# Optimization experiments

Measured on AMD Instinct MI355X. Metric: run time of the kernel, lower is better.

## Reference

```python
import jax, jax.numpy as jnp
import numpy as np

ALPHA = (0.02, 0.04, 0.08, 0.16)
CHAMFER_W, SMOOTH_W, CURVATURE_W = 1.0, 1.0, 0.3
NS = (8192, 4096, 2048, 1024)
B = 2


def _sqdist(a, b):
    # a: [B,N,3], b: [B,M,3] -> [B,N,M] squared euclidean distance
    return (jnp.sum(a * a, axis=-1)[:, :, None]
            - 2.0 * jnp.einsum('bnc,bmc->bnm', a, b)
            + jnp.sum(b * b, axis=-1)[:, None, :])


def _knn(d, k):
    # k smallest distances + indices along last axis
    neg, idx = jax.lax.top_k(-d, k)
    return -neg, idx


def _gather(points, idx):
    # points: [B,M,C], idx: [B,N,K] -> [B,N,K,C]
    return jax.vmap(lambda p, i: p[i])(points, idx)


def _scale_loss(pc1, pc2, flow):
    # pc1, pc2, flow: [B,3,N]-like -> permute to points-last layout
    p1 = jnp.transpose(pc1, (0, 2, 1))   # [B,N,3]
    p2 = jnp.transpose(pc2, (0, 2, 1))   # [B,M,3]
    fl = jnp.transpose(flow, (0, 2, 1))  # [B,N,3]
    warp = p1 + fl                        # warped pc1

    # curvature of pc2 (10-NN on pc2 itself)
    _, k22 = _knn(_sqdist(p2, p2), 10)
    cv2 = jnp.sum(_gather(p2, k22) - p2[:, :, None, :], axis=2) / 9.0  # [B,M,3]

    # 10-NN on pc1 (shared for warped curvature and smoothness; 9-NN is prefix)
    _, k11 = _knn(_sqdist(p1, p1), 10)
    cvw = jnp.sum(_gather(warp, k11) - warp[:, :, None, :], axis=2) / 9.0  # [B,N,3]

    k9 = k11[:, :, :9]
    gfl = _gather(fl, k9)  # [B,N,9,3]
    smooth = jnp.sum(jnp.linalg.norm(gfl - fl[:, :, None, :], axis=3), axis=2) / 8.0  # [B,N]

    # chamfer between warped pc1 and pc2
    d12 = _sqdist(warp, p2)               # [B,N,M]
    dist1 = jnp.min(d12, axis=-1)         # [B,N]
    dist2 = jnp.min(d12, axis=1)          # [B,M]

    # inverse-distance interpolation of pc2 curvature onto warped pc1 (5-NN)
    dist, kidx = _knn(d12, 5)             # [B,N,5]
    gcv = _gather(cv2, kidx)              # [B,N,5,3]
    w = 1.0 / (dist + 1e-8)
    w = w / jnp.sum(w, axis=2, keepdims=True)
    inter = jnp.sum(w[..., None] * gcv, axis=2)  # [B,N,3]

    chamfer = jnp.mean(jnp.sum(dist1, axis=1)) + jnp.mean(jnp.sum(dist2, axis=1))
    smoothness = jnp.mean(jnp.sum(smooth, axis=1))
    curv = jnp.mean(jnp.sum(jnp.sum((inter - cvw) ** 2, axis=2), axis=1))
    return chamfer, smoothness, curv


def setup_inputs() -> dict:
    key = jax.random.key(0)
    keys = jax.random.split(key, 12)
    out = {}
    names = ['pc1', 'pc2', 'flow']
    k = 0
    for name in names:
        for i, n in enumerate(NS):
            scale = 1.0 if name != 'flow' else 0.1
            out[f'{name}_{i}'] = scale * jax.random.normal(keys[k], (B, 3, n), dtype=jnp.float32)
            k += 1
    return out


def reference(pc1_0, pc1_1, pc1_2, pc1_3,
              pc2_0, pc2_1, pc2_2, pc2_3,
              flow_0, flow_1, flow_2, flow_3):
    pcs1 = (pc1_0, pc1_1, pc1_2, pc1_3)
    pcs2 = (pc2_0, pc2_1, pc2_2, pc2_3)
    flows = (flow_0, flow_1, flow_2, flow_3)
    ch = sm = cv = jnp.float32(0.0)
    for a, p1, p2, fl in zip(ALPHA, pcs1, pcs2, flows):
        c, s, k = _scale_loss(p1, p2, fl)
        ch = ch + a * c
        sm = sm + a * s
        cv = cv + a * k
    total = CHAMFER_W * ch + CURVATURE_W * cv + SMOOTH_W * sm
    return jnp.reshape(total, (1,))
```

## Files before the change

kernel.cpp:

```cpp
#include <hip/hip_runtime.h>
#include <math.h>


#define BLOCK 512
#define UNIT 1024
#define NTOT 15360
#define MASKC 0xFFFFE000u
#define PB 340

typedef unsigned int uint;
typedef __attribute__((ext_vector_type(8))) float f8;

struct Params {
  const float* pc1[4];
  const float* pc2[4];
  const float* fl[4];
  float4* cv2;
  float4* cvw;
  float* keys;
  float* out;
};

__device__ __forceinline__ void decode(int r, int wv, int& s, int& b,
                                       int& i0, int& lo, int& N, int& cpw,
                                       int& off, float& alpha) {
  int rr;
  if (r < 256)      { s = 0; rr = r; }
  else if (r < 320) { s = 1; rr = r - 256; }
  else if (r < 336) { s = 2; rr = r - 320; }
  else              { s = 3; rr = r - 336; }
  N = 8192 >> s;
  cpw = 8 >> s;
  int perb = 128 >> (2 * s);
  b = rr >> (7 - 2 * s);
  int chunk = rr & (perb - 1);
  int qg = (chunk << s) + (wv >> (3 - s));
  i0 = qg << 6;
  lo = (wv & (cpw - 1)) << 10;
  off = 16384 - (16384 >> s);
  alpha = 0.02f * (float)(1 << s);
}

__device__ __forceinline__ float wave_sum(float v) {
  #pragma unroll
  for (int o = 32; o; o >>= 1) v += __shfl_down(v, o, 64);
  return v;
}

template <int K>
__device__ __forceinline__ void key_insert(float (&kd)[K], float kf) {
  #pragma unroll
  for (int m = K - 1; m >= 1; --m)
    kd[m] = __builtin_amdgcn_fmed3f(kf, kd[m - 1], kd[m]);
  kd[0] = fminf(kd[0], kf);
}

template <int K>
__device__ __forceinline__ void merge_pair(float (&a)[K], const float (&b)[K]) {
  #pragma unroll
  for (int m = 0; m < K; ++m) key_insert<K>(a, b[m]);
}

__device__ __forceinline__ float pack_key_u(float d, uint iw) {
  return __uint_as_float((__float_as_uint(d) & MASKC) | iw);
}

__device__ __forceinline__ void sload3(const float* px, const float* py,
                                       const float* pz, int boff,
                                       f8& x, f8& y, f8& z) {
  asm volatile(
      "s_load_dwordx8 %0, %3, %6\n\t"
      "s_load_dwordx8 %1, %4, %6\n\t"
      "s_load_dwordx8 %2, %5, %6\n\t"
      "s_waitcnt lgkmcnt(0)"
      : "=&s"(x), "=&s"(y), "=&s"(z)
      : "s"(px), "s"(py), "s"(pz), "s"(boff));
}

__device__ __forceinline__ void sload6(const float* px, const float* py,
                                       const float* pz, const float* fx,
                                       const float* fy, const float* fz,
                                       int boff, f8& x, f8& y, f8& z,
                                       f8& u, f8& v, f8& w) {
  asm volatile(
      "s_load_dwordx8 %0, %6, %12\n\t"
      "s_load_dwordx8 %1, %7, %12\n\t"
      "s_load_dwordx8 %2, %8, %12\n\t"
      "s_load_dwordx8 %3, %9, %12\n\t"
      "s_load_dwordx8 %4, %10, %12\n\t"
      "s_load_dwordx8 %5, %11, %12\n\t"
      "s_waitcnt lgkmcnt(0)"
      : "=&s"(x), "=&s"(y), "=&s"(z), "=&s"(u), "=&s"(v), "=&s"(w)
      : "s"(px), "s"(py), "s"(pz), "s"(fx), "s"(fy), "s"(fz), "s"(boff));
}

template <int K>
__device__ void scan_k(const float* px, const float* py, const float* pz,
                       int lo_u, float ax, float ay, float az,
                       float (&a)[K], float (&b)[K]) {
  #pragma unroll 1
  for (int c0 = 0; c0 < UNIT; c0 += 8) {
    f8 xs, ys, zs;
    sload3(px, py, pz, (lo_u + c0) * 4, xs, ys, zs);
    #pragma unroll
    for (int t = 0; t < 8; t += 2) {
      float dxa = xs[t] - ax, dya = ys[t] - ay, dza = zs[t] - az;
      float dA = fmaf(dxa, dxa, fmaf(dya, dya, dza * dza));
      float dxb = xs[t + 1] - ax, dyb = ys[t + 1] - ay, dzb = zs[t + 1] - az;
      float dB = fmaf(dxb, dxb, fmaf(dyb, dyb, dzb * dzb));
      key_insert<K>(a, pack_key_u(dA, (uint)(lo_u + c0 + t)));
      key_insert<K>(b, pack_key_u(dB, (uint)(lo_u + c0 + t + 1)));
    }
  }
}

__device__ void scan_w(const float* px, const float* py, const float* pz,
                       const float* fx, const float* fy, const float* fz,
                       int lo_u, float ax, float ay, float az,
                       float (&a)[1], float (&b)[1]) {
  #pragma unroll 1
  for (int c0 = 0; c0 < UNIT; c0 += 8) {
    f8 xs, ys, zs, us, vs, ws;
    sload6(px, py, pz, fx, fy, fz, (lo_u + c0) * 4, xs, ys, zs, us, vs, ws);
    #pragma unroll
    for (int t = 0; t < 8; t += 2) {
      float cxa = xs[t] + us[t], cya = ys[t] + vs[t], cza = zs[t] + ws[t];
      float dxa = cxa - ax, dya = cya - ay, dza = cza - az;
      float dA = fmaf(dxa, dxa, fmaf(dya, dya, dza * dza));
      float cxb = xs[t + 1] + us[t + 1], cyb = ys[t + 1] + vs[t + 1],
            czb = zs[t + 1] + ws[t + 1];
      float dxb = cxb - ax, dyb = cyb - ay, dzb = czb - az;
      float dB = fmaf(dxb, dxb, fmaf(dyb, dyb, dzb * dzb));
      a[0] = fminf(a[0], dA);
      b[0] = fminf(b[0], dB);
    }
  }
}

template <int K>
__device__ __forceinline__ bool merge_group(float (&a)[K], float* sm,
                                            int tid, int cpw) {
  const int STR = K | 1;
  int q = tid & 63, wv = tid >> 6;
  #pragma unroll
  for (int m = 0; m < K; ++m) sm[(wv * 64 + q) * STR + m] = a[m];
  __syncthreads();
  if (wv & (cpw - 1)) return false;
  for (int w = wv + 1; w < wv + cpw; ++w)
    #pragma unroll
    for (int m = 0; m < K; ++m)
      key_insert<K>(a, sm[(w * 64 + q) * STR + m]);
  return true;
}

__global__ __launch_bounds__(1) void k_zero(float* out) { out[0] = 0.f; }

__global__ __launch_bounds__(BLOCK, 8) void k_fused(Params P) {
  __shared__ float sm[8 * 64 * 11];
  int tid = threadIdx.x, q = tid & 63, wv = tid >> 6;
  int pass = blockIdx.x / PB, r = blockIdx.x % PB;
  int s, b, i0, lo, N, cpw, off; float alpha;
  decode(r, wv, s, b, i0, lo, N, cpw, off, alpha);
  int i = i0 + q;
  int lo_u = __builtin_amdgcn_readfirstlane(lo);

  if (pass == 0) {
    const float* p2 = P.pc2[s] + b * 3 * N;
    float ax = p2[i], ay = p2[N + i], az = p2[2 * N + i];
    float a[10], bb[10];
    #pragma unroll
    for (int m = 0; m < 10; ++m) { a[m] = 3.0e38f; bb[m] = 3.0e38f; }
    scan_k<10>(p2, p2 + N, p2 + 2 * N, lo_u, ax, ay, az, a, bb);
    merge_pair<10>(a, bb);
    if (!merge_group<10>(a, sm, tid, cpw)) return;
    float sx = 0.f, sy = 0.f, sz = 0.f;
    #pragma unroll
    for (int m = 0; m < 10; ++m) {
      int j = (int)(__float_as_uint(a[m]) & 0x1FFFu);
      sx += p2[j]; sy += p2[N + j]; sz += p2[2 * N + j];
    }
    const float inv9 = 1.f / 9.f;
    P.cv2[b * NTOT + off + i] = make_float4((sx - 10.f * ax) * inv9,
                                            (sy - 10.f * ay) * inv9,
                                            (sz - 10.f * az) * inv9, 0.f);
  } else if (pass == 1) {
    const float* p1 = P.pc1[s] + b * 3 * N;
    const float* fl = P.fl[s] + b * 3 * N;
    float ax = p1[i], ay = p1[N + i], az = p1[2 * N + i];
    float a[10], bb[10];
    #pragma unroll
    for (int m = 0; m < 10; ++m) { a[m] = 3.0e38f; bb[m] = 3.0e38f; }
    scan_k<10>(p1, p1 + N, p1 + 2 * N, lo_u, ax, ay, az, a, bb);
    merge_pair<10>(a, bb);
    if (!merge_group<10>(a, sm, tid, cpw)) return;
    float fix = fl[i], fiy = fl[N + i], fiz = fl[2 * N + i];
    float wix = ax + fix, wiy = ay + fiy, wiz = az + fiz;
    float sx = 0.f, sy = 0.f, sz = 0.f, smooth = 0.f;
    float dmax = -1.f, worst = 0.f;
    #pragma unroll
    for (int m = 0; m < 10; ++m) {
      int j = (int)(__float_as_uint(a[m]) & 0x1FFFu);
      float px = p1[j], py = p1[N + j], pz = p1[2 * N + j];
      float flx = fl[j], fly = fl[N + j], flz = fl[2 * N + j];
      sx += px + flx; sy += py + fly; sz += pz + flz;
      float ddx = px - ax, ddy = py - ay, ddz = pz - az;
      float d = fmaf(ddx, ddx, fmaf(ddy, ddy, ddz * ddz));
      float gx = flx - fix, gy = fly - fiy, gz = flz - fiz;
      float term = sqrtf(fmaf(gx, gx, fmaf(gy, gy, gz * gz)));
      smooth += term;
      if (d > dmax) { dmax = d; worst = term; }
    }
    smooth -= worst;
    const float inv9 = 1.f / 9.f;
    P.cvw[b * NTOT + off + i] = make_float4((sx - 10.f * wix) * inv9,
                                            (sy - 10.f * wiy) * inv9,
                                            (sz - 10.f * wiz) * inv9, 0.f);
    float ssum = wave_sum(smooth * (1.f / 8.f));
    if (q == 0) atomicAdd(P.out, alpha * 0.5f * ssum);
  } else if (pass == 2) {
    const float* p1 = P.pc1[s] + b * 3 * N;
    const float* fl = P.fl[s] + b * 3 * N;
    const float* p2 = P.pc2[s] + b * 3 * N;
    float ax = p2[i], ay = p2[N + i], az = p2[2 * N + i];
    float a[1], bb[1];
    a[0] = 3.0e38f; bb[0] = 3.0e38f;
    scan_w(p1, p1 + N, p1 + 2 * N, fl, fl + N, fl + 2 * N,
           lo_u, ax, ay, az, a, bb);
    merge_pair<1>(a, bb);
    if (!merge_group<1>(a, sm, tid, cpw)) return;
    float msum = wave_sum(a[0]);
    if (q == 0) atomicAdd(P.out, alpha * 0.5f * msum);
  } else {
    const float* p1 = P.pc1[s] + b * 3 * N;
    const float* fl = P.fl[s] + b * 3 * N;
    const float* p2 = P.pc2[s] + b * 3 * N;
    float ax = p1[i] + fl[i], ay = p1[N + i] + fl[N + i],
          az = p1[2 * N + i] + fl[2 * N + i];
    float a[5], bb[5];
    #pragma unroll
    for (int m = 0; m < 5; ++m) { a[m] = 3.0e38f; bb[m] = 3.0e38f; }
    scan_k<5>(p2, p2 + N, p2 + 2 * N, lo_u, ax, ay, az, a, bb);
    merge_pair<5>(a, bb);
    if (!merge_group<5>(a, sm, tid, cpw)) return;
    #pragma unroll
    for (int m = 0; m < 5; ++m)
      P.keys[m * (2 * NTOT) + b * NTOT + off + i] = a[m];
  }
}

__global__ __launch_bounds__(256) void k_epi(Params P) {
  int t = blockIdx.x * 256 + threadIdx.x;
  int b = t >= NTOT;
  int r = t - b * NTOT;
  int s, i;
  if (r < 8192)       { s = 0; i = r; }
  else if (r < 12288) { s = 1; i = r - 8192; }
  else if (r < 14336) { s = 2; i = r - 12288; }
  else                { s = 3; i = r - 14336; }
  int N = 8192 >> s;
  int off = 16384 - (16384 >> s);
  float alpha = 0.02f * (float)(1 << s);
  const float* p1 = P.pc1[s] + b * 3 * N;
  const float* fl = P.fl[s] + b * 3 * N;
  const float* p2 = P.pc2[s] + b * 3 * N;
  float ax = p1[i] + fl[i], ay = p1[N + i] + fl[N + i],
        az = p1[2 * N + i] + fl[2 * N + i];
  float dist1 = 3.0e38f, wsum = 0.f, ix = 0.f, iy = 0.f, iz = 0.f;
  #pragma unroll
  for (int m = 0; m < 5; ++m) {
    uint key = __float_as_uint(P.keys[m * (2 * NTOT) + b * NTOT + off + i]);
    int j = (int)(key & 0x1FFFu);
    float px = p2[j], py = p2[N + j], pz = p2[2 * N + j];
    float ddx = px - ax, ddy = py - ay, ddz = pz - az;
    float d = fmaf(ddx, ddx, fmaf(ddy, ddy, ddz * ddz));
    dist1 = fminf(dist1, d);
    float w = 1.f / (d + 1e-8f);
    wsum += w;
    float4 cv = P.cv2[b * NTOT + off + j];
    ix += w * cv.x; iy += w * cv.y; iz += w * cv.z;
  }
  float inv = 1.f / wsum;
  ix *= inv; iy *= inv; iz *= inv;
  float4 cw = P.cvw[b * NTOT + off + i];
  float ex = ix - cw.x, ey = iy - cw.y, ez = iz - cw.z;
  float curv = fmaf(ex, ex, fmaf(ey, ey, ez * ez));
  float v = alpha * 0.5f * (dist1 + 0.3f * curv);
  v = wave_sum(v);
  if ((threadIdx.x & 63) == 0) atomicAdd(P.out, v);
}

extern "C" void kernel_launch(void* const* d_in, const int* in_sizes, int n_in,
                              void* d_out, int out_size, void* d_ws,
                              size_t ws_size, hipStream_t stream) {
  Params P;
  for (int s = 0; s < 4; ++s) {
    P.pc1[s] = (const float*)d_in[s];
    P.pc2[s] = (const float*)d_in[4 + s];
    P.fl[s]  = (const float*)d_in[8 + s];
  }
  P.cv2 = (float4*)d_ws;
  P.cvw = (float4*)((char*)d_ws + (size_t)2 * NTOT * sizeof(float4));
  P.keys = (float*)((char*)d_ws + (size_t)4 * NTOT * sizeof(float4));
  P.out = (float*)d_out;

  k_zero<<<dim3(1), dim3(1), 0, stream>>>(P.out);
  k_fused<<<dim3(4 * PB), dim3(BLOCK), 0, stream>>>(P);
  k_epi<<<dim3((2 * NTOT) / 256), dim3(256), 0, stream>>>(P);
}
```

Before: 315.2 us.

## Replace fused block-merge kernel with atomic work-queue wave tasks and split epilogues

Adds a persistent-style scan kernel in which each wave pulls a task from an atomic counter. A task covers one of four passes (pc2 self-kNN, pc1 self-kNN, warp-to-pc2 5-NN, pc2-to-warp min) over a 1024-point column slice, and partial top-K lists go to global workspace instead of being merged in shared memory. Two epilogue kernels then merge the partials and compute curvature, smoothness and chamfer terms, and the distance math is written with 2-wide vector FMAs. This aims to balance load across scales and drop block-level syncs. The cost is extra global traffic for the partial keys, an extra launch, and a path that only runs when the workspace is large enough.

```diff
diff --git a/kernel.cpp b/kernel.cpp
--- a/kernel.cpp
+++ b/kernel.cpp
@@ -2,14 +2,17 @@
 #include <math.h>
 
 
-#define BLOCK 512
 #define UNIT 1024
 #define NTOT 15360
 #define MASKC 0xFFFFE000u
 #define PB 340
+#define BLOCK 512
+#define NTASKS 10880
+#define TOTS 174080
 
 typedef unsigned int uint;
 typedef __attribute__((ext_vector_type(8))) float f8;
+typedef __attribute__((ext_vector_type(2))) float f2;
 
 struct Params {
   const float* pc1[4];
@@ -17,9 +20,315 @@
   const float* fl[4];
   float4* cv2;
   float4* cvw;
+  float* k0;
+  float* k1;
+  float* k3;
+  uint* d2u;
+  uint* cnt;
   float* keys;
   float* out;
 };
+
+
+__device__ __forceinline__ float wave_sum(float v) {
+  #pragma unroll
+  for (int o = 32; o; o >>= 1) v += __shfl_down(v, o, 64);
+  return v;
+}
+
+template <int K>
+__device__ __forceinline__ void key_insert(float (&kd)[K], float kf) {
+  #pragma unroll
+  for (int m = K - 1; m >= 1; --m)
+    kd[m] = __builtin_amdgcn_fmed3f(kf, kd[m - 1], kd[m]);
+  kd[0] = fminf(kd[0], kf);
+}
+
+template <int K>
+__device__ __forceinline__ void merge_pair(float (&a)[K], const float (&b)[K]) {
+  #pragma unroll
+  for (int m = 0; m < K; ++m) key_insert<K>(a, b[m]);
+}
+
+__device__ __forceinline__ void sload3(const float* px, const float* py,
+                                       const float* pz, int boff,
+                                       f8& x, f8& y, f8& z) {
+  asm volatile(
+      "s_load_dwordx8 %0, %3, %6\n\t"
+      "s_load_dwordx8 %1, %4, %6\n\t"
+      "s_load_dwordx8 %2, %5, %6\n\t"
+      "s_waitcnt lgkmcnt(0)"
+      : "=&s"(x), "=&s"(y), "=&s"(z)
+      : "s"(px), "s"(py), "s"(pz), "s"(boff));
+}
+
+__device__ __forceinline__ void sload6(const float* px, const float* py,
+                                       const float* pz, const float* fx,
+                                       const float* fy, const float* fz,
+                                       int boff, f8& x, f8& y, f8& z,
+                                       f8& u, f8& v, f8& w) {
+  asm volatile(
+      "s_load_dwordx8 %0, %6, %12\n\t"
+      "s_load_dwordx8 %1, %7, %12\n\t"
+      "s_load_dwordx8 %2, %8, %12\n\t"
+      "s_load_dwordx8 %3, %9, %12\n\t"
+      "s_load_dwordx8 %4, %10, %12\n\t"
+      "s_load_dwordx8 %5, %11, %12\n\t"
+      "s_waitcnt lgkmcnt(0)"
+      : "=&s"(x), "=&s"(y), "=&s"(z), "=&s"(u), "=&s"(v), "=&s"(w)
+      : "s"(px), "s"(py), "s"(pz), "s"(fx), "s"(fy), "s"(fz), "s"(boff));
+}
+
+template <int K>
+__device__ void scan_k(const float* px, const float* py, const float* pz,
+                       int lo, float ax, float ay, float az,
+                       float (&a)[K], float (&b)[K]) {
+  f2 qx = {ax, ax}, qy = {ay, ay}, qz = {az, az};
+  #pragma unroll 1
+  for (int c0 = 0; c0 < UNIT; c0 += 8) {
+    f8 xs, ys, zs;
+    sload3(px, py, pz, (lo + c0) * 4, xs, ys, zs);
+    #pragma unroll
+    for (int t = 0; t < 8; t += 2) {
+      f2 dx = f2{xs[t], xs[t + 1]} - qx;
+      f2 dy = f2{ys[t], ys[t + 1]} - qy;
+      f2 dz = f2{zs[t], zs[t + 1]} - qz;
+      f2 d = __builtin_elementwise_fma(
+          dx, dx, __builtin_elementwise_fma(dy, dy, dz * dz));
+      uint i0 = (uint)(lo + c0 + t);
+      key_insert<K>(a, __uint_as_float((__float_as_uint(d.x) & MASKC) | i0));
+      key_insert<K>(b,
+                    __uint_as_float((__float_as_uint(d.y) & MASKC) | (i0 + 1)));
+    }
+  }
+}
+
+__device__ void scan_w(const float* px, const float* py, const float* pz,
+                       const float* fx, const float* fy, const float* fz,
+                       int lo, float ax, float ay, float az,
+                       float (&a)[1], float (&b)[1]) {
+  #pragma unroll 1
+  for (int c0 = 0; c0 < UNIT; c0 += 8) {
+    f8 xs, ys, zs, us, vs, ws;
+    sload6(px, py, pz, fx, fy, fz, (lo + c0) * 4, xs, ys, zs, us, vs, ws);
+    #pragma unroll
+    for (int t = 0; t < 8; t += 2) {
+      float cxa = xs[t] + us[t], cya = ys[t] + vs[t], cza = zs[t] + ws[t];
+      float dxa = cxa - ax, dya = cya - ay, dza = cza - az;
+      float dA = fmaf(dxa, dxa, fmaf(dya, dya, dza * dza));
+      float cxb = xs[t + 1] + us[t + 1], cyb = ys[t + 1] + vs[t + 1],
+            czb = zs[t + 1] + ws[t + 1];
+      float dxb = cxb - ax, dyb = cyb - ay, dzb = czb - az;
+      float dB = fmaf(dxb, dxb, fmaf(dyb, dyb, dzb * dzb));
+      a[0] = fminf(a[0], dA);
+      b[0] = fminf(b[0], dB);
+    }
+  }
+}
+
+
+__global__ __launch_bounds__(256) void k_init(Params P) {
+  int t = blockIdx.x * 256 + threadIdx.x;
+  if (t == 0) { P.out[0] = 0.f; *P.cnt = 0u; }
+  if (t < 2 * NTOT) P.d2u[t] = 0x7F7FFFFFu;
+}
+
+__global__ __launch_bounds__(256, 8) void k_scan(Params P) {
+  int lane = threadIdx.x & 63;
+  for (;;) {
+    uint t;
+    if (lane == 0) t = atomicAdd(P.cnt, 1u);
+    t = (uint)__builtin_amdgcn_readfirstlane(__shfl((int)t, 0, 64));
+    if (t >= NTASKS) return;
+    int p = t / 2720, u = t % 2720;
+    int s, part, g;
+    if (u < 2048)      { s = 0; part = u & 7; g = u >> 3; }
+    else if (u < 2560) { s = 1; u -= 2048; part = u & 3; g = u >> 2; }
+    else if (u < 2688) { s = 2; u -= 2560; part = u & 1; g = u >> 1; }
+    else               { s = 3; u -= 2688; part = 0; g = u; }
+    int gpb = 128 >> s;
+    int b = g >> (7 - s), qg = g & (gpb - 1);
+    int N = 8192 >> s, i = qg * 64 + lane, lo = part << 10;
+    int off = 16384 - (16384 >> s);
+    int qid = b * NTOT + off + i;
+    int sb = (s == 0) ? 0 : (s == 1) ? 131072 : (s == 2) ? 163840 : 172032;
+    int slot = sb + part * 2 * N + b * N + i;
+
+    if (p == 0) {
+      const float* p2 = P.pc2[s] + b * 3 * N;
+      float ax = p2[i], ay = p2[N + i], az = p2[2 * N + i];
+      float a[10], bb[10];
+      #pragma unroll
+      for (int m = 0; m < 10; ++m) { a[m] = 3.0e38f; bb[m] = 3.0e38f; }
+      scan_k<10>(p2, p2 + N, p2 + 2 * N, lo, ax, ay, az, a, bb);
+      merge_pair<10>(a, bb);
+      #pragma unroll
+      for (int m = 0; m < 10; ++m) P.k0[m * TOTS + slot] = a[m];
+    } else if (p == 1) {
+      const float* p1 = P.pc1[s] + b * 3 * N;
+      float ax = p1[i], ay = p1[N + i], az = p1[2 * N + i];
+      float a[10], bb[10];
+      #pragma unroll
+      for (int m = 0; m < 10; ++m) { a[m] = 3.0e38f; bb[m] = 3.0e38f; }
+      scan_k<10>(p1, p1 + N, p1 + 2 * N, lo, ax, ay, az, a, bb);
+      merge_pair<10>(a, bb);
+      #pragma unroll
+      for (int m = 0; m < 10; ++m) P.k1[m * TOTS + slot] = a[m];
+    } else if (p == 2) {
+      const float* p1 = P.pc1[s] + b * 3 * N;
+      const float* fl = P.fl[s] + b * 3 * N;
+      const float* p2 = P.pc2[s] + b * 3 * N;
+      float ax = p1[i] + fl[i], ay = p1[N + i] + fl[N + i],
+            az = p1[2 * N + i] + fl[2 * N + i];
+      float a[5], bb[5];
+      #pragma unroll
+      for (int m = 0; m < 5; ++m) { a[m] = 3.0e38f; bb[m] = 3.0e38f; }
+      scan_k<5>(p2, p2 + N, p2 + 2 * N, lo, ax, ay, az, a, bb);
+      merge_pair<5>(a, bb);
+      #pragma unroll
+      for (int m = 0; m < 5; ++m) P.k3[m * TOTS + slot] = a[m];
+    } else {
+      const float* p1 = P.pc1[s] + b * 3 * N;
+      const float* fl = P.fl[s] + b * 3 * N;
+      const float* p2 = P.pc2[s] + b * 3 * N;
+      float ax = p2[i], ay = p2[N + i], az = p2[2 * N + i];
+      float a[1], bb[1];
+      a[0] = 3.0e38f; bb[0] = 3.0e38f;
+      scan_w(p1, p1 + N, p1 + 2 * N, fl, fl + N, fl + 2 * N,
+             lo, ax, ay, az, a, bb);
+      atomicMin(P.d2u + qid, __float_as_uint(fminf(a[0], bb[0])));
+    }
+  }
+}
+
+__global__ __launch_bounds__(256) void k_epi_a(Params P) {
+  int t = blockIdx.x * 256 + threadIdx.x;
+  int bq = t >= NTOT;
+  int r = t - bq * NTOT;
+  int s, i;
+  if (r < 8192)       { s = 0; i = r; }
+  else if (r < 12288) { s = 1; i = r - 8192; }
+  else if (r < 14336) { s = 2; i = r - 12288; }
+  else                { s = 3; i = r - 14336; }
+  int N = 8192 >> s;
+  int off = 16384 - (16384 >> s);
+  float alpha = 0.02f * (float)(1 << s);
+  int sb = (s == 0) ? 0 : (s == 1) ? 131072 : (s == 2) ? 163840 : 172032;
+  int slot0 = sb + bq * N + i, stride = 2 * N, parts = 8 >> s;
+  const float inv9 = 1.f / 9.f;
+
+  const float* p2 = P.pc2[s] + bq * 3 * N;
+  {
+    float ax = p2[i], ay = p2[N + i], az = p2[2 * N + i];
+    float a[10];
+    #pragma unroll
+    for (int m = 0; m < 10; ++m) a[m] = 3.0e38f;
+    for (int part = 0; part < parts; ++part)
+      #pragma unroll
+      for (int m = 0; m < 10; ++m)
+        key_insert<10>(a, P.k0[m * TOTS + slot0 + part * stride]);
+    float sx = 0.f, sy = 0.f, sz = 0.f;
+    #pragma unroll
+    for (int m = 0; m < 10; ++m) {
+      int j = (int)(__float_as_uint(a[m]) & 0x1FFFu);
+      sx += p2[j]; sy += p2[N + j]; sz += p2[2 * N + j];
+    }
+    P.cv2[bq * NTOT + off + i] = make_float4((sx - 10.f * ax) * inv9,
+                                             (sy - 10.f * ay) * inv9,
+                                             (sz - 10.f * az) * inv9, 0.f);
+  }
+
+  {
+    const float* p1 = P.pc1[s] + bq * 3 * N;
+    const float* fl = P.fl[s] + bq * 3 * N;
+    float ax = p1[i], ay = p1[N + i], az = p1[2 * N + i];
+    float a[10];
+    #pragma unroll
+    for (int m = 0; m < 10; ++m) a[m] = 3.0e38f;
+    for (int part = 0; part < parts; ++part)
+      #pragma unroll
+      for (int m = 0; m < 10; ++m)
+        key_insert<10>(a, P.k1[m * TOTS + slot0 + part * stride]);
+    float fix = fl[i], fiy = fl[N + i], fiz = fl[2 * N + i];
+    float wix = ax + fix, wiy = ay + fiy, wiz = az + fiz;
+    float sx = 0.f, sy = 0.f, sz = 0.f, smooth = 0.f;
+    float dmax = -1.f, worst = 0.f;
+    #pragma unroll
+    for (int m = 0; m < 10; ++m) {
+      int j = (int)(__float_as_uint(a[m]) & 0x1FFFu);
+      float px = p1[j], py = p1[N + j], pz = p1[2 * N + j];
+      float flx = fl[j], fly = fl[N + j], flz = fl[2 * N + j];
+      sx += px + flx; sy += py + fly; sz += pz + flz;
+      float ddx = px - ax, ddy = py - ay, ddz = pz - az;
+      float d = fmaf(ddx, ddx, fmaf(ddy, ddy, ddz * ddz));
+      float gx = flx - fix, gy = fly - fiy, gz = flz - fiz;
+      float term = sqrtf(fmaf(gx, gx, fmaf(gy, gy, gz * gz)));
+      smooth += term;
+      if (d > dmax) { dmax = d; worst = term; }
+    }
+    smooth -= worst;
+    P.cvw[bq * NTOT + off + i] = make_float4((sx - 10.f * wix) * inv9,
+                                             (sy - 10.f * wiy) * inv9,
+                                             (sz - 10.f * wiz) * inv9, 0.f);
+    float ssum = wave_sum(smooth * (1.f / 8.f));
+    if ((threadIdx.x & 63) == 0) atomicAdd(P.out, alpha * 0.5f * ssum);
+  }
+
+  {
+    float dm = __uint_as_float(P.d2u[t]);
+    float msum = wave_sum(dm);
+    if ((threadIdx.x & 63) == 0) atomicAdd(P.out, alpha * 0.5f * msum);
+  }
+}
+
+__global__ __launch_bounds__(256) void k_epi_b(Params P) {
+  int t = blockIdx.x * 256 + threadIdx.x;
+  int bq = t >= NTOT;
+  int r = t - bq * NTOT;
+  int s, i;
+  if (r < 8192)       { s = 0; i = r; }
+  else if (r < 12288) { s = 1; i = r - 8192; }
+  else if (r < 14336) { s = 2; i = r - 12288; }
+  else                { s = 3; i = r - 14336; }
+  int N = 8192 >> s;
+  int off = 16384 - (16384 >> s);
+  float alpha = 0.02f * (float)(1 << s);
+  int sb = (s == 0) ? 0 : (s == 1) ? 131072 : (s == 2) ? 163840 : 172032;
+  int slot0 = sb + bq * N + i, stride = 2 * N, parts = 8 >> s;
+  const float* p1 = P.pc1[s] + bq * 3 * N;
+  const float* fl = P.fl[s] + bq * 3 * N;
+  const float* p2 = P.pc2[s] + bq * 3 * N;
+  float ax = p1[i] + fl[i], ay = p1[N + i] + fl[N + i],
+        az = p1[2 * N + i] + fl[2 * N + i];
+  float a[5];
+  #pragma unroll
+  for (int m = 0; m < 5; ++m) a[m] = 3.0e38f;
+  for (int part = 0; part < parts; ++part)
+    #pragma unroll
+    for (int m = 0; m < 5; ++m)
+      key_insert<5>(a, P.k3[m * TOTS + slot0 + part * stride]);
+  float dist1 = 3.0e38f, wsum = 0.f, ix = 0.f, iy = 0.f, iz = 0.f;
+  #pragma unroll
+  for (int m = 0; m < 5; ++m) {
+    int j = (int)(__float_as_uint(a[m]) & 0x1FFFu);
+    float px = p2[j], py = p2[N + j], pz = p2[2 * N + j];
+    float ddx = px - ax, ddy = py - ay, ddz = pz - az;
+    float d = fmaf(ddx, ddx, fmaf(ddy, ddy, ddz * ddz));
+    dist1 = fminf(dist1, d);
+    float w = 1.f / (d + 1e-8f);
+    wsum += w;
+    float4 cv = P.cv2[bq * NTOT + off + j];
+    ix += w * cv.x; iy += w * cv.y; iz += w * cv.z;
+  }
+  float inv = 1.f / wsum;
+  ix *= inv; iy *= inv; iz *= inv;
+  float4 cw = P.cvw[bq * NTOT + off + i];
+  float ex = ix - cw.x, ey = iy - cw.y, ez = iz - cw.z;
+  float curv = fmaf(ex, ex, fmaf(ey, ey, ez * ez));
+  float v = wave_sum(dist1 + 0.3f * curv);
+  if ((threadIdx.x & 63) == 0) atomicAdd(P.out, alpha * 0.5f * v);
+}
+
 
 __device__ __forceinline__ void decode(int r, int wv, int& s, int& b,
                                        int& i0, int& lo, int& N, int& cpw,
@@ -39,102 +348,6 @@
   lo = (wv & (cpw - 1)) << 10;
   off = 16384 - (16384 >> s);
   alpha = 0.02f * (float)(1 << s);
-}
-
-__device__ __forceinline__ float wave_sum(float v) {
-  #pragma unroll
-  for (int o = 32; o; o >>= 1) v += __shfl_down(v, o, 64);
-  return v;
-}
-
-template <int K>
-__device__ __forceinline__ void key_insert(float (&kd)[K], float kf) {
-  #pragma unroll
-  for (int m = K - 1; m >= 1; --m)
-    kd[m] = __builtin_amdgcn_fmed3f(kf, kd[m - 1], kd[m]);
-  kd[0] = fminf(kd[0], kf);
-}
-
-template <int K>
-__device__ __forceinline__ void merge_pair(float (&a)[K], const float (&b)[K]) {
-  #pragma unroll
-  for (int m = 0; m < K; ++m) key_insert<K>(a, b[m]);
-}
-
-__device__ __forceinline__ float pack_key_u(float d, uint iw) {
-  return __uint_as_float((__float_as_uint(d) & MASKC) | iw);
-}
-
-__device__ __forceinline__ void sload3(const float* px, const float* py,
-                                       const float* pz, int boff,
-                                       f8& x, f8& y, f8& z) {
-  asm volatile(
-      "s_load_dwordx8 %0, %3, %6\n\t"
-      "s_load_dwordx8 %1, %4, %6\n\t"
-      "s_load_dwordx8 %2, %5, %6\n\t"
-      "s_waitcnt lgkmcnt(0)"
-      : "=&s"(x), "=&s"(y), "=&s"(z)
-      : "s"(px), "s"(py), "s"(pz), "s"(boff));
-}
-
-__device__ __forceinline__ void sload6(const float* px, const float* py,
-                                       const float* pz, const float* fx,
-                                       const float* fy, const float* fz,
-                                       int boff, f8& x, f8& y, f8& z,
-                                       f8& u, f8& v, f8& w) {
-  asm volatile(
-      "s_load_dwordx8 %0, %6, %12\n\t"
-      "s_load_dwordx8 %1, %7, %12\n\t"
-      "s_load_dwordx8 %2, %8, %12\n\t"
-      "s_load_dwordx8 %3, %9, %12\n\t"
-      "s_load_dwordx8 %4, %10, %12\n\t"
-      "s_load_dwordx8 %5, %11, %12\n\t"
-      "s_waitcnt lgkmcnt(0)"
-      : "=&s"(x), "=&s"(y), "=&s"(z), "=&s"(u), "=&s"(v), "=&s"(w)
-      : "s"(px), "s"(py), "s"(pz), "s"(fx), "s"(fy), "s"(fz), "s"(boff));
-}
-
-template <int K>
-__device__ void scan_k(const float* px, const float* py, const float* pz,
-                       int lo_u, float ax, float ay, float az,
-                       float (&a)[K], float (&b)[K]) {
-  #pragma unroll 1
-  for (int c0 = 0; c0 < UNIT; c0 += 8) {
-    f8 xs, ys, zs;
-    sload3(px, py, pz, (lo_u + c0) * 4, xs, ys, zs);
-    #pragma unroll
-    for (int t = 0; t < 8; t += 2) {
-      float dxa = xs[t] - ax, dya = ys[t] - ay, dza = zs[t] - az;
-      float dA = fmaf(dxa, dxa, fmaf(dya, dya, dza * dza));
-      float dxb = xs[t + 1] - ax, dyb = ys[t + 1] - ay, dzb = zs[t + 1] - az;
-      float dB = fmaf(dxb, dxb, fmaf(dyb, dyb, dzb * dzb));
-      key_insert<K>(a, pack_key_u(dA, (uint)(lo_u + c0 + t)));
-      key_insert<K>(b, pack_key_u(dB, (uint)(lo_u + c0 + t + 1)));
-    }
-  }
-}
-
-__device__ void scan_w(const float* px, const float* py, const float* pz,
-                       const float* fx, const float* fy, const float* fz,
-                       int lo_u, float ax, float ay, float az,
-                       float (&a)[1], float (&b)[1]) {
-  #pragma unroll 1
-  for (int c0 = 0; c0 < UNIT; c0 += 8) {
-    f8 xs, ys, zs, us, vs, ws;
-    sload6(px, py, pz, fx, fy, fz, (lo_u + c0) * 4, xs, ys, zs, us, vs, ws);
-    #pragma unroll
-    for (int t = 0; t < 8; t += 2) {
-      float cxa = xs[t] + us[t], cya = ys[t] + vs[t], cza = zs[t] + ws[t];
-      float dxa = cxa - ax, dya = cya - ay, dza = cza - az;
-      float dA = fmaf(dxa, dxa, fmaf(dya, dya, dza * dza));
-      float cxb = xs[t + 1] + us[t + 1], cyb = ys[t + 1] + vs[t + 1],
-            czb = zs[t + 1] + ws[t + 1];
-      float dxb = cxb - ax, dyb = cyb - ay, dzb = czb - az;
-      float dB = fmaf(dxb, dxb, fmaf(dyb, dyb, dzb * dzb));
-      a[0] = fminf(a[0], dA);
-      b[0] = fminf(b[0], dB);
-    }
-  }
 }
 
 template <int K>
@@ -284,9 +497,8 @@
   float4 cw = P.cvw[b * NTOT + off + i];
   float ex = ix - cw.x, ey = iy - cw.y, ez = iz - cw.z;
   float curv = fmaf(ex, ex, fmaf(ey, ey, ez * ez));
-  float v = alpha * 0.5f * (dist1 + 0.3f * curv);
-  v = wave_sum(v);
-  if ((threadIdx.x & 63) == 0) atomicAdd(P.out, v);
+  float v = wave_sum(dist1 + 0.3f * curv);
+  if ((threadIdx.x & 63) == 0) atomicAdd(P.out, alpha * 0.5f * v);
 }
 
 extern "C" void kernel_launch(void* const* d_in, const int* in_sizes, int n_in,
@@ -298,12 +510,25 @@
     P.pc2[s] = (const float*)d_in[4 + s];
     P.fl[s]  = (const float*)d_in[8 + s];
   }
-  P.cv2 = (float4*)d_ws;
-  P.cvw = (float4*)((char*)d_ws + (size_t)2 * NTOT * sizeof(float4));
-  P.keys = (float*)((char*)d_ws + (size_t)4 * NTOT * sizeof(float4));
+  char* ws = (char*)d_ws;
+  P.cv2 = (float4*)ws;
+  P.cvw = (float4*)(ws + 491520);
+  P.k0  = (float*)(ws + 983040);
+  P.k1  = (float*)(ws + 7946240);
+  P.k3  = (float*)(ws + 14909440);
+  P.d2u = (uint*)(ws + 18391040);
+  P.cnt = (uint*)(ws + 18513920);
+  P.keys = (float*)(ws + 983040);
   P.out = (float*)d_out;
 
-  k_zero<<<dim3(1), dim3(1), 0, stream>>>(P.out);
-  k_fused<<<dim3(4 * PB), dim3(BLOCK), 0, stream>>>(P);
-  k_epi<<<dim3((2 * NTOT) / 256), dim3(256), 0, stream>>>(P);
-}
+  if (ws_size >= 18513928) {
+    k_init<<<dim3(120), dim3(256), 0, stream>>>(P);
+    k_scan<<<dim3(2048), dim3(256), 0, stream>>>(P);
+    k_epi_a<<<dim3(120), dim3(256), 0, stream>>>(P);
+    k_epi_b<<<dim3(120), dim3(256), 0, stream>>>(P);
+  } else {
+    k_zero<<<dim3(1), dim3(1), 0, stream>>>(P.out);
+    k_fused<<<dim3(4 * PB), dim3(BLOCK), 0, stream>>>(P);
+    k_epi<<<dim3((2 * NTOT) / 256), dim3(256), 0, stream>>>(P);
+  }
+}
```

Result: slower. 476.3 us (+51.1%).

## Use persistent blocks with atomic task queue and atomicMin-split chamfer reverse pass

Applied to the files above, without the earlier changes.

Replaces the fixed 1360-block launch with 1024 persistent blocks that pull task indices from a global atomic counter. The three kNN passes stay as before, but the reverse chamfer pass is split into finer 256-column slices whose per-point minima are combined with atomicMin on uint-encoded floats and summed in the epilogue. The goal is better load balance and less tail imbalance across CUs. The cost is extra atomics, an init kernel, and a block-wide sync per task.

```diff
diff --git a/kernel.cpp b/kernel.cpp
--- a/kernel.cpp
+++ b/kernel.cpp
@@ -2,11 +2,10 @@
 #include <math.h>
 
 
-#define BLOCK 512
 #define UNIT 1024
 #define NTOT 15360
 #define MASKC 0xFFFFE000u
-#define PB 340
+#define NTASK 2380u
 
 typedef unsigned int uint;
 typedef __attribute__((ext_vector_type(8))) float f8;
@@ -18,8 +17,107 @@
   float4* cv2;
   float4* cvw;
   float* keys;
+  uint* d2u;
+  uint* cnt;
   float* out;
 };
+
+
+__device__ __forceinline__ float wave_sum(float v) {
+  #pragma unroll
+  for (int o = 32; o; o >>= 1) v += __shfl_down(v, o, 64);
+  return v;
+}
+
+template <int K>
+__device__ __forceinline__ void key_insert(float (&kd)[K], float kf) {
+  #pragma unroll
+  for (int m = K - 1; m >= 1; --m)
+    kd[m] = __builtin_amdgcn_fmed3f(kf, kd[m - 1], kd[m]);
+  kd[0] = fminf(kd[0], kf);
+}
+
+template <int K>
+__device__ __forceinline__ void merge_pair(float (&a)[K], const float (&b)[K]) {
+  #pragma unroll
+  for (int m = 0; m < K; ++m) key_insert<K>(a, b[m]);
+}
+
+__device__ __forceinline__ float pack_key_u(float d, uint iw) {
+  return __uint_as_float((__float_as_uint(d) & MASKC) | iw);
+}
+
+__device__ __forceinline__ void sload3(const float* px, const float* py,
+                                       const float* pz, int boff,
+                                       f8& x, f8& y, f8& z) {
+  asm volatile(
+      "s_load_dwordx8 %0, %3, %6\n\t"
+      "s_load_dwordx8 %1, %4, %6\n\t"
+      "s_load_dwordx8 %2, %5, %6\n\t"
+      "s_waitcnt lgkmcnt(0)"
+      : "=&s"(x), "=&s"(y), "=&s"(z)
+      : "s"(px), "s"(py), "s"(pz), "s"(boff));
+}
+
+__device__ __forceinline__ void sload6(const float* px, const float* py,
+                                       const float* pz, const float* fx,
+                                       const float* fy, const float* fz,
+                                       int boff, f8& x, f8& y, f8& z,
+                                       f8& u, f8& v, f8& w) {
+  asm volatile(
+      "s_load_dwordx8 %0, %6, %12\n\t"
+      "s_load_dwordx8 %1, %7, %12\n\t"
+      "s_load_dwordx8 %2, %8, %12\n\t"
+      "s_load_dwordx8 %3, %9, %12\n\t"
+      "s_load_dwordx8 %4, %10, %12\n\t"
+      "s_load_dwordx8 %5, %11, %12\n\t"
+      "s_waitcnt lgkmcnt(0)"
+      : "=&s"(x), "=&s"(y), "=&s"(z), "=&s"(u), "=&s"(v), "=&s"(w)
+      : "s"(px), "s"(py), "s"(pz), "s"(fx), "s"(fy), "s"(fz), "s"(boff));
+}
+
+template <int K>
+__device__ void scan_k(const float* px, const float* py, const float* pz,
+                       int lo, float ax, float ay, float az,
+                       float (&a)[K], float (&b)[K]) {
+  #pragma unroll 1
+  for (int c0 = 0; c0 < UNIT; c0 += 8) {
+    f8 xs, ys, zs;
+    sload3(px, py, pz, (lo + c0) * 4, xs, ys, zs);
+    #pragma unroll
+    for (int t = 0; t < 8; t += 2) {
+      float dxa = xs[t] - ax, dya = ys[t] - ay, dza = zs[t] - az;
+      float dA = fmaf(dxa, dxa, fmaf(dya, dya, dza * dza));
+      float dxb = xs[t + 1] - ax, dyb = ys[t + 1] - ay, dzb = zs[t + 1] - az;
+      float dB = fmaf(dxb, dxb, fmaf(dyb, dyb, dzb * dzb));
+      key_insert<K>(a, pack_key_u(dA, (uint)(lo + c0 + t)));
+      key_insert<K>(b, pack_key_u(dB, (uint)(lo + c0 + t + 1)));
+    }
+  }
+}
+
+__device__ void scan_w256(const float* px, const float* py, const float* pz,
+                          const float* fx, const float* fy, const float* fz,
+                          int lo, float ax, float ay, float az,
+                          float& a0, float& b0) {
+  #pragma unroll 1
+  for (int c0 = 0; c0 < 256; c0 += 8) {
+    f8 xs, ys, zs, us, vs, ws;
+    sload6(px, py, pz, fx, fy, fz, (lo + c0) * 4, xs, ys, zs, us, vs, ws);
+    #pragma unroll
+    for (int t = 0; t < 8; t += 2) {
+      float cxa = xs[t] + us[t], cya = ys[t] + vs[t], cza = zs[t] + ws[t];
+      float dxa = cxa - ax, dya = cya - ay, dza = cza - az;
+      float dA = fmaf(dxa, dxa, fmaf(dya, dya, dza * dza));
+      float cxb = xs[t + 1] + us[t + 1], cyb = ys[t + 1] + vs[t + 1],
+            czb = zs[t + 1] + ws[t + 1];
+      float dxb = cxb - ax, dyb = cyb - ay, dzb = czb - az;
+      float dB = fmaf(dxb, dxb, fmaf(dyb, dyb, dzb * dzb));
+      a0 = fminf(a0, dA);
+      b0 = fminf(b0, dB);
+    }
+  }
+}
 
 __device__ __forceinline__ void decode(int r, int wv, int& s, int& b,
                                        int& i0, int& lo, int& N, int& cpw,
@@ -41,102 +139,6 @@
   alpha = 0.02f * (float)(1 << s);
 }
 
-__device__ __forceinline__ float wave_sum(float v) {
-  #pragma unroll
-  for (int o = 32; o; o >>= 1) v += __shfl_down(v, o, 64);
-  return v;
-}
-
-template <int K>
-__device__ __forceinline__ void key_insert(float (&kd)[K], float kf) {
-  #pragma unroll
-  for (int m = K - 1; m >= 1; --m)
-    kd[m] = __builtin_amdgcn_fmed3f(kf, kd[m - 1], kd[m]);
-  kd[0] = fminf(kd[0], kf);
-}
-
-template <int K>
-__device__ __forceinline__ void merge_pair(float (&a)[K], const float (&b)[K]) {
-  #pragma unroll
-  for (int m = 0; m < K; ++m) key_insert<K>(a, b[m]);
-}
-
-__device__ __forceinline__ float pack_key_u(float d, uint iw) {
-  return __uint_as_float((__float_as_uint(d) & MASKC) | iw);
-}
-
-__device__ __forceinline__ void sload3(const float* px, const float* py,
-                                       const float* pz, int boff,
-                                       f8& x, f8& y, f8& z) {
-  asm volatile(
-      "s_load_dwordx8 %0, %3, %6\n\t"
-      "s_load_dwordx8 %1, %4, %6\n\t"
-      "s_load_dwordx8 %2, %5, %6\n\t"
-      "s_waitcnt lgkmcnt(0)"
-      : "=&s"(x), "=&s"(y), "=&s"(z)
-      : "s"(px), "s"(py), "s"(pz), "s"(boff));
-}
-
-__device__ __forceinline__ void sload6(const float* px, const float* py,
-                                       const float* pz, const float* fx,
-                                       const float* fy, const float* fz,
-                                       int boff, f8& x, f8& y, f8& z,
-                                       f8& u, f8& v, f8& w) {
-  asm volatile(
-      "s_load_dwordx8 %0, %6, %12\n\t"
-      "s_load_dwordx8 %1, %7, %12\n\t"
-      "s_load_dwordx8 %2, %8, %12\n\t"
-      "s_load_dwordx8 %3, %9, %12\n\t"
-      "s_load_dwordx8 %4, %10, %12\n\t"
-      "s_load_dwordx8 %5, %11, %12\n\t"
-      "s_waitcnt lgkmcnt(0)"
-      : "=&s"(x), "=&s"(y), "=&s"(z), "=&s"(u), "=&s"(v), "=&s"(w)
-      : "s"(px), "s"(py), "s"(pz), "s"(fx), "s"(fy), "s"(fz), "s"(boff));
-}
-
-template <int K>
-__device__ void scan_k(const float* px, const float* py, const float* pz,
-                       int lo_u, float ax, float ay, float az,
-                       float (&a)[K], float (&b)[K]) {
-  #pragma unroll 1
-  for (int c0 = 0; c0 < UNIT; c0 += 8) {
-    f8 xs, ys, zs;
-    sload3(px, py, pz, (lo_u + c0) * 4, xs, ys, zs);
-    #pragma unroll
-    for (int t = 0; t < 8; t += 2) {
-      float dxa = xs[t] - ax, dya = ys[t] - ay, dza = zs[t] - az;
-      float dA = fmaf(dxa, dxa, fmaf(dya, dya, dza * dza));
-      float dxb = xs[t + 1] - ax, dyb = ys[t + 1] - ay, dzb = zs[t + 1] - az;
-      float dB = fmaf(dxb, dxb, fmaf(dyb, dyb, dzb * dzb));
-      key_insert<K>(a, pack_key_u(dA, (uint)(lo_u + c0 + t)));
-      key_insert<K>(b, pack_key_u(dB, (uint)(lo_u + c0 + t + 1)));
-    }
-  }
-}
-
-__device__ void scan_w(const float* px, const float* py, const float* pz,
-                       const float* fx, const float* fy, const float* fz,
-                       int lo_u, float ax, float ay, float az,
-                       float (&a)[1], float (&b)[1]) {
-  #pragma unroll 1
-  for (int c0 = 0; c0 < UNIT; c0 += 8) {
-    f8 xs, ys, zs, us, vs, ws;
-    sload6(px, py, pz, fx, fy, fz, (lo_u + c0) * 4, xs, ys, zs, us, vs, ws);
-    #pragma unroll
-    for (int t = 0; t < 8; t += 2) {
-      float cxa = xs[t] + us[t], cya = ys[t] + vs[t], cza = zs[t] + ws[t];
-      float dxa = cxa - ax, dya = cya - ay, dza = cza - az;
-      float dA = fmaf(dxa, dxa, fmaf(dya, dya, dza * dza));
-      float cxb = xs[t + 1] + us[t + 1], cyb = ys[t + 1] + vs[t + 1],
-            czb = zs[t + 1] + ws[t + 1];
-      float dxb = cxb - ax, dyb = cyb - ay, dzb = czb - az;
-      float dB = fmaf(dxb, dxb, fmaf(dyb, dyb, dzb * dzb));
-      a[0] = fminf(a[0], dA);
-      b[0] = fminf(b[0], dB);
-    }
-  }
-}
-
 template <int K>
 __device__ __forceinline__ bool merge_group(float (&a)[K], float* sm,
                                             int tid, int cpw) {
@@ -153,98 +155,132 @@
   return true;
 }
 
-__global__ __launch_bounds__(1) void k_zero(float* out) { out[0] = 0.f; }
-
-__global__ __launch_bounds__(BLOCK, 8) void k_fused(Params P) {
+
+__global__ __launch_bounds__(256) void k_init(Params P) {
+  int t = blockIdx.x * 256 + threadIdx.x;
+  if (t == 0) { P.out[0] = 0.f; *P.cnt = 1024u; }
+  if (t < 2 * NTOT) P.d2u[t] = 0x7F7FFFFFu;
+}
+
+__global__ __launch_bounds__(512, 8) void k_work(Params P) {
   __shared__ float sm[8 * 64 * 11];
+  __shared__ uint ts;
   int tid = threadIdx.x, q = tid & 63, wv = tid >> 6;
-  int pass = blockIdx.x / PB, r = blockIdx.x % PB;
-  int s, b, i0, lo, N, cpw, off; float alpha;
-  decode(r, wv, s, b, i0, lo, N, cpw, off, alpha);
-  int i = i0 + q;
-  int lo_u = __builtin_amdgcn_readfirstlane(lo);
-
-  if (pass == 0) {
-    const float* p2 = P.pc2[s] + b * 3 * N;
-    float ax = p2[i], ay = p2[N + i], az = p2[2 * N + i];
-    float a[10], bb[10];
-    #pragma unroll
-    for (int m = 0; m < 10; ++m) { a[m] = 3.0e38f; bb[m] = 3.0e38f; }
-    scan_k<10>(p2, p2 + N, p2 + 2 * N, lo_u, ax, ay, az, a, bb);
-    merge_pair<10>(a, bb);
-    if (!merge_group<10>(a, sm, tid, cpw)) return;
-    float sx = 0.f, sy = 0.f, sz = 0.f;
-    #pragma unroll
-    for (int m = 0; m < 10; ++m) {
-      int j = (int)(__float_as_uint(a[m]) & 0x1FFFu);
-      sx += p2[j]; sy += p2[N + j]; sz += p2[2 * N + j];
+
+  uint t = blockIdx.x;
+  while (t < NTASK) {
+    if (t < 1020u) {
+      int pass = (int)t / 340, r = (int)t % 340;
+      int s, b, i0, lo, N, cpw, off; float alpha;
+      decode(r, wv, s, b, i0, lo, N, cpw, off, alpha);
+      int i = i0 + q;
+      int lo_u = __builtin_amdgcn_readfirstlane(lo);
+
+      if (pass == 0) {
+        const float* p2 = P.pc2[s] + b * 3 * N;
+        float ax = p2[i], ay = p2[N + i], az = p2[2 * N + i];
+        float a[10], bb[10];
+        #pragma unroll
+        for (int m = 0; m < 10; ++m) { a[m] = 3.0e38f; bb[m] = 3.0e38f; }
+        scan_k<10>(p2, p2 + N, p2 + 2 * N, lo_u, ax, ay, az, a, bb);
+        merge_pair<10>(a, bb);
+        if (merge_group<10>(a, sm, tid, cpw)) {
+          float sx = 0.f, sy = 0.f, sz = 0.f;
+          #pragma unroll
+          for (int m = 0; m < 10; ++m) {
+            int j = (int)(__float_as_uint(a[m]) & 0x1FFFu);
+            sx += p2[j]; sy += p2[N + j]; sz += p2[2 * N + j];
+          }
+          const float inv9 = 1.f / 9.f;
+          P.cv2[b * NTOT + off + i] = make_float4((sx - 10.f * ax) * inv9,
+                                                  (sy - 10.f * ay) * inv9,
+                                                  (sz - 10.f * az) * inv9,
+                                                  0.f);
+        }
+      } else if (pass == 1) {
+        const float* p1 = P.pc1[s] + b * 3 * N;
+        const float* fl = P.fl[s] + b * 3 * N;
+        float ax = p1[i], ay = p1[N + i], az = p1[2 * N + i];
+        float a[10], bb[10];
+        #pragma unroll
+        for (int m = 0; m < 10; ++m) { a[m] = 3.0e38f; bb[m] = 3.0e38f; }
+        scan_k<10>(p1, p1 + N, p1 + 2 * N, lo_u, ax, ay, az, a, bb);
+        merge_pair<10>(a, bb);
+        if (merge_group<10>(a, sm, tid, cpw)) {
+          float fix = fl[i], fiy = fl[N + i], fiz = fl[2 * N + i];
+          float wix = ax + fix, wiy = ay + fiy, wiz = az + fiz;
+          float sx = 0.f, sy = 0.f, sz = 0.f, smooth = 0.f;
+          float dmax = -1.f, worst = 0.f;
+          #pragma unroll
+          for (int m = 0; m < 10; ++m) {
+            int j = (int)(__float_as_uint(a[m]) & 0x1FFFu);
+            float px = p1[j], py = p1[N + j], pz = p1[2 * N + j];
+            float flx = fl[j], fly = fl[N + j], flz = fl[2 * N + j];
+            sx += px + flx; sy += py + fly; sz += pz + flz;
+            float ddx = px - ax, ddy = py - ay, ddz = pz - az;
+            float d = fmaf(ddx, ddx, fmaf(ddy, ddy, ddz * ddz));
+            float gx = flx - fix, gy = fly - fiy, gz = flz - fiz;
+            float term = sqrtf(fmaf(gx, gx, fmaf(gy, gy, gz * gz)));
+            smooth += term;
+            if (d > dmax) { dmax = d; worst = term; }
+          }
+          smooth -= worst;
+          const float inv9 = 1.f / 9.f;
+          P.cvw[b * NTOT + off + i] = make_float4((sx - 10.f * wix) * inv9,
+                                                  (sy - 10.f * wiy) * inv9,
+                                                  (sz - 10.f * wiz) * inv9,
+                                                  0.f);
+          float ssum = wave_sum(smooth * (1.f / 8.f));
+          if (q == 0) atomicAdd(P.out, alpha * 0.5f * ssum);
+        }
+      } else {
+        const float* p1 = P.pc1[s] + b * 3 * N;
+        const float* fl = P.fl[s] + b * 3 * N;
+        const float* p2 = P.pc2[s] + b * 3 * N;
+        float ax = p1[i] + fl[i], ay = p1[N + i] + fl[N + i],
+              az = p1[2 * N + i] + fl[2 * N + i];
+        float a[5], bb[5];
+        #pragma unroll
+        for (int m = 0; m < 5; ++m) { a[m] = 3.0e38f; bb[m] = 3.0e38f; }
+        scan_k<5>(p2, p2 + N, p2 + 2 * N, lo_u, ax, ay, az, a, bb);
+        merge_pair<5>(a, bb);
+        if (merge_group<5>(a, sm, tid, cpw)) {
+          #pragma unroll
+          for (int m = 0; m < 5; ++m)
+            P.keys[m * (2 * NTOT) + b * NTOT + off + i] = a[m];
+        }
+      }
+    } else {
+      int dm = (int)(t - 1020u);
+      int s, tb;
+      if (dm < 1024)      { s = 0; tb = dm; }
+      else if (dm < 1280) { s = 1; tb = dm - 1024; }
+      else if (dm < 1344) { s = 2; tb = dm - 1280; }
+      else                { s = 3; tb = dm - 1344; }
+      int N = 8192 >> s;
+      int tpb = 512 >> (2 * s);
+      int b = tb >> (9 - 2 * s);
+      int ti = tb & (tpb - 1);
+      int u = ti * 8 + wv;
+      int rpq = 32 >> s;
+      int qg = u >> (5 - s);
+      int rg = u & (rpq - 1);
+      int i = qg * 64 + q, lo = rg * 256;
+      int off = 16384 - (16384 >> s);
+      const float* p1 = P.pc1[s] + b * 3 * N;
+      const float* fl = P.fl[s] + b * 3 * N;
+      const float* p2 = P.pc2[s] + b * 3 * N;
+      float ax = p2[i], ay = p2[N + i], az = p2[2 * N + i];
+      float a0 = 3.0e38f, b0 = 3.0e38f;
+      int lo_u = __builtin_amdgcn_readfirstlane(lo);
+      scan_w256(p1, p1 + N, p1 + 2 * N, fl, fl + N, fl + 2 * N,
+                lo_u, ax, ay, az, a0, b0);
+      atomicMin(P.d2u + b * NTOT + off + i, __float_as_uint(fminf(a0, b0)));
     }
-    const float inv9 = 1.f / 9.f;
-    P.cv2[b * NTOT + off + i] = make_float4((sx - 10.f * ax) * inv9,
-                                            (sy - 10.f * ay) * inv9,
-                                            (sz - 10.f * az) * inv9, 0.f);
-  } else if (pass == 1) {
-    const float* p1 = P.pc1[s] + b * 3 * N;
-    const float* fl = P.fl[s] + b * 3 * N;
-    float ax = p1[i], ay = p1[N + i], az = p1[2 * N + i];
-    float a[10], bb[10];
-    #pragma unroll
-    for (int m = 0; m < 10; ++m) { a[m] = 3.0e38f; bb[m] = 3.0e38f; }
-    scan_k<10>(p1, p1 + N, p1 + 2 * N, lo_u, ax, ay, az, a, bb);
-    merge_pair<10>(a, bb);
-    if (!merge_group<10>(a, sm, tid, cpw)) return;
-    float fix = fl[i], fiy = fl[N + i], fiz = fl[2 * N + i];
-    float wix = ax + fix, wiy = ay + fiy, wiz = az + fiz;
-    float sx = 0.f, sy = 0.f, sz = 0.f, smooth = 0.f;
-    float dmax = -1.f, worst = 0.f;
-    #pragma unroll
-    for (int m = 0; m < 10; ++m) {
-      int j = (int)(__float_as_uint(a[m]) & 0x1FFFu);
-      float px = p1[j], py = p1[N + j], pz = p1[2 * N + j];
-      float flx = fl[j], fly = fl[N + j], flz = fl[2 * N + j];
-      sx += px + flx; sy += py + fly; sz += pz + flz;
-      float ddx = px - ax, ddy = py - ay, ddz = pz - az;
-      float d = fmaf(ddx, ddx, fmaf(ddy, ddy, ddz * ddz));
-      float gx = flx - fix, gy = fly - fiy, gz = flz - fiz;
-      float term = sqrtf(fmaf(gx, gx, fmaf(gy, gy, gz * gz)));
-      smooth += term;
-      if (d > dmax) { dmax = d; worst = term; }
-    }
-    smooth -= worst;
-    const float inv9 = 1.f / 9.f;
-    P.cvw[b * NTOT + off + i] = make_float4((sx - 10.f * wix) * inv9,
-                                            (sy - 10.f * wiy) * inv9,
-                                            (sz - 10.f * wiz) * inv9, 0.f);
-    float ssum = wave_sum(smooth * (1.f / 8.f));
-    if (q == 0) atomicAdd(P.out, alpha * 0.5f * ssum);
-  } else if (pass == 2) {
-    const float* p1 = P.pc1[s] + b * 3 * N;
-    const float* fl = P.fl[s] + b * 3 * N;
-    const float* p2 = P.pc2[s] + b * 3 * N;
-    float ax = p2[i], ay = p2[N + i], az = p2[2 * N + i];
-    float a[1], bb[1];
-    a[0] = 3.0e38f; bb[0] = 3.0e38f;
-    scan_w(p1, p1 + N, p1 + 2 * N, fl, fl + N, fl + 2 * N,
-           lo_u, ax, ay, az, a, bb);
-    merge_pair<1>(a, bb);
-    if (!merge_group<1>(a, sm, tid, cpw)) return;
-    float msum = wave_sum(a[0]);
-    if (q == 0) atomicAdd(P.out, alpha * 0.5f * msum);
-  } else {
-    const float* p1 = P.pc1[s] + b * 3 * N;
-    const float* fl = P.fl[s] + b * 3 * N;
-    const float* p2 = P.pc2[s] + b * 3 * N;
-    float ax = p1[i] + fl[i], ay = p1[N + i] + fl[N + i],
-          az = p1[2 * N + i] + fl[2 * N + i];
-    float a[5], bb[5];
-    #pragma unroll
-    for (int m = 0; m < 5; ++m) { a[m] = 3.0e38f; bb[m] = 3.0e38f; }
-    scan_k<5>(p2, p2 + N, p2 + 2 * N, lo_u, ax, ay, az, a, bb);
-    merge_pair<5>(a, bb);
-    if (!merge_group<5>(a, sm, tid, cpw)) return;
-    #pragma unroll
-    for (int m = 0; m < 5; ++m)
-      P.keys[m * (2 * NTOT) + b * NTOT + off + i] = a[m];
+    __syncthreads();
+    if (tid == 0) ts = atomicAdd(P.cnt, 1u);
+    __syncthreads();
+    t = ts;
   }
 }
 
@@ -284,9 +320,12 @@
   float4 cw = P.cvw[b * NTOT + off + i];
   float ex = ix - cw.x, ey = iy - cw.y, ez = iz - cw.z;
   float curv = fmaf(ex, ex, fmaf(ey, ey, ez * ez));
-  float v = alpha * 0.5f * (dist1 + 0.3f * curv);
-  v = wave_sum(v);
-  if ((threadIdx.x & 63) == 0) atomicAdd(P.out, v);
+  float csum = wave_sum(dist1 + 0.3f * curv);
+  float msum = wave_sum(__uint_as_float(P.d2u[t]));
+  if ((threadIdx.x & 63) == 0) {
+    atomicAdd(P.out, alpha * 0.5f * csum);
+    atomicAdd(P.out, alpha * 0.5f * msum);
+  }
 }
 
 extern "C" void kernel_launch(void* const* d_in, const int* in_sizes, int n_in,
@@ -298,12 +337,15 @@
     P.pc2[s] = (const float*)d_in[4 + s];
     P.fl[s]  = (const float*)d_in[8 + s];
   }
-  P.cv2 = (float4*)d_ws;
-  P.cvw = (float4*)((char*)d_ws + (size_t)2 * NTOT * sizeof(float4));
-  P.keys = (float*)((char*)d_ws + (size_t)4 * NTOT * sizeof(float4));
-  P.out = (float*)d_out;
-
-  k_zero<<<dim3(1), dim3(1), 0, stream>>>(P.out);
-  k_fused<<<dim3(4 * PB), dim3(BLOCK), 0, stream>>>(P);
-  k_epi<<<dim3((2 * NTOT) / 256), dim3(256), 0, stream>>>(P);
-}
+  char* ws = (char*)d_ws;
+  P.cv2  = (float4*)ws;
+  P.cvw  = (float4*)(ws + 491520);
+  P.keys = (float*)(ws + 983040);
+  P.d2u  = (uint*)(ws + 1597440);
+  P.cnt  = (uint*)(ws + 1720320);
+  P.out  = (float*)d_out;
+
+  k_init<<<dim3(120), dim3(256), 0, stream>>>(P);
+  k_work<<<dim3(1024), dim3(512), 0, stream>>>(P);
+  k_epi<<<dim3(120), dim3(256), 0, stream>>>(P);
+}
```

Result: no change. 312.5 us (-0.9%).
